# Kernel optimization log

Hardware: AMD Instinct MI355X
Metric: run time of the kernel (lower is better)

The kernel has to match this reference:

```python
import jax, jax.numpy as jnp
import numpy as np

B, QL, DL, RSZ, T = 16, 32, 12, 500, 2
DW, DH = 256, 512
HP = DH // 2  # per-direction GRU hidden
NW, NE = 50000, 100000


def _gru_dir(xp, mask, Wh, bh, reverse):
    # xp: [B, L, 3H'] precomputed input projections; mask: [B, L, 1]
    Hp = Wh.shape[1]
    xp_t = jnp.swapaxes(xp, 0, 1)
    m_t = jnp.swapaxes(mask, 0, 1)
    h0 = jnp.zeros((xp.shape[0], Hp), xp.dtype)

    def step(h, inp):
        x, m = inp
        gh = h @ Wh.T + bh
        r = jax.nn.sigmoid(x[:, :Hp] + gh[:, :Hp])
        z = jax.nn.sigmoid(x[:, Hp:2 * Hp] + gh[:, Hp:2 * Hp])
        n = jnp.tanh(x[:, 2 * Hp:] + r * gh[:, 2 * Hp:])
        hn = (1.0 - z) * n + z * h
        h = m * hn + (1.0 - m) * h  # skip updates at pad tokens
        return h, h

    hT, hs = jax.lax.scan(step, h0, (xp_t, m_t), reverse=reverse)
    return jnp.swapaxes(hs, 0, 1), hT


def _bigru(tokens, emb, Wx, Wh, bx, bh):
    # tokens: [B, L] int, 0 = pad. Wx: [2, 3H', D], Wh: [2, 3H', H'], bx/bh: [2, 3H']
    x = emb[tokens]
    mask = (tokens != 0).astype(x.dtype)[..., None]
    xp_f = jnp.einsum('bld,gd->blg', x, Wx[0]) + bx[0]
    xp_b = jnp.einsum('bld,gd->blg', x, Wx[1]) + bx[1]
    hs_f, hT_f = _gru_dir(xp_f, mask, Wh[0], bh[0], False)
    hs_b, hT_b = _gru_dir(xp_b, mask, Wh[1], bh[1], True)
    word_h = jnp.concatenate([hs_f, hs_b], -1) * mask  # zero pad positions
    sent = jnp.concatenate([hT_f, hT_b], -1)  # last fwd / last bwd hidden
    return word_h, sent


def setup_inputs() -> dict:
    key = jax.random.key(0)
    ks = jax.random.split(key, 12)

    def gru_p(k, din):
        k1, k2 = jax.random.split(k, 2)
        s = 1.0 / float(np.sqrt(HP))
        return (jax.random.normal(k1, (2, 3 * HP, din), jnp.float32) * s,
                jax.random.normal(k2, (2, 3 * HP, HP), jnp.float32) * s,
                jnp.zeros((2, 3 * HP), jnp.float32),
                jnp.zeros((2, 3 * HP), jnp.float32))

    q_Wx, q_Wh, q_bx, q_bh = gru_p(ks[0], DW)
    d_Wx, d_Wh, d_bx, d_bh = gru_p(ks[1], DW)
    kaim = float(np.sqrt(2.0 / DH))
    return {
        'questions': jax.random.randint(ks[2], (B, QL), 0, NW),
        'e_s': jax.random.uniform(ks[3], (B, NE), jnp.float32),
        'pair': jax.random.randint(ks[4], (T, B, RSZ, 2), 0, NE),
        'desc': jax.random.randint(ks[5], (T, B, RSZ, DL), 0, NW),
        'word_emb': jax.random.normal(ks[6], (NW, DW), jnp.float32) * 0.02,
        'q_Wx': q_Wx, 'q_Wh': q_Wh, 'q_bx': q_bx, 'q_bh': q_bh,
        'd_Wx': d_Wx, 'd_Wh': d_Wh, 'd_bx': d_bx, 'd_bh': d_bh,
        'step_W': jax.random.normal(ks[7], (T, DH, DH), jnp.float32) * kaim,
        'step_b': jnp.zeros((T, DH), jnp.float32),
        'rel_W': jax.random.normal(ks[8], (1, DH), jnp.float32) * kaim,
        'rel_b': jnp.zeros((1,), jnp.float32),
        'qcls_W': jax.random.normal(ks[9], (NE, DH), jnp.float32) * kaim,
        'qcls_b': jnp.zeros((NE,), jnp.float32),
    }


def reference(questions, e_s, pair, desc, word_emb, q_Wx, q_Wh, q_bx, q_bh,
              d_Wx, d_Wh, d_bx, d_bh, step_W, step_b, rel_W, rel_b, qcls_W, qcls_b):
    q_word_h, q_emb = _bigru(questions, word_emb, q_Wx, q_Wh, q_bx, q_bh)
    bsz, num_ent = e_s.shape
    last_e = e_s
    for t in range(pair.shape[0]):  # num_steps hops (small, fixed)
        cq = jnp.tanh(q_emb @ step_W[t].T + step_b[t])              # [B,H]
        q_dist = jax.nn.softmax(jnp.einsum('bh,blh->bl', cq, q_word_h), axis=1)
        ctx = jnp.einsum('bl,blh->bh', q_dist, q_word_h)            # [B,H]
        d_tok = desc[t].reshape(-1, desc.shape[-1])                 # [B*rsz, L]
        _, d_emb = _bigru(d_tok, word_emb, d_Wx, d_Wh, d_bx, d_bh)
        d_emb = d_emb.reshape(bsz, -1, d_emb.shape[-1])             # [B,rsz,H]
        d_logit = jnp.einsum('bh,brh,h->br', ctx, d_emb, rel_W[0]) + rel_b[0]
        d_prob = jax.nn.sigmoid(d_logit)                            # [B,rsz]
        sub, obj = pair[t, :, :, 0], pair[t, :, :, 1]
        obj_p = jnp.take_along_axis(last_e, sub, axis=1) * d_prob   # follow: gather
        last_e = jax.vmap(lambda o, p: jnp.zeros((num_ent,), e_s.dtype).at[o].add(p))(obj, obj_p)
        z = jax.lax.stop_gradient(jnp.where(last_e > 1.0, last_e, 1.0))
        last_e = last_e / z
    q_mask = jax.nn.sigmoid(q_emb @ qcls_W.T + qcls_b)
    return last_e * q_mask
```

## Files before the change

kernel.cpp:

```cpp
#include <hip/hip_runtime.h>
#include <math.h>

#define B_    16
#define QL_   32
#define DL_   12
#define RSZ_  500
#define T_    2
#define DW_   256
#define DH_   512
#define HP_   256
#define NW_   50000
#define NE_   100000
#define NSEQD (T_*B_*RSZ_)
#define MDESC 64
#define NBLK_DESC 500
#define NBLK_FUSED 502

typedef _Float16 half8 __attribute__((ext_vector_type(8)));
typedef float   floatx4 __attribute__((ext_vector_type(4)));

__device__ __forceinline__ float sigf(float x){
  return __builtin_amdgcn_rcpf(1.0f + __expf(-x));
}
__device__ __forceinline__ float tanhfast(float x){
  return 1.0f - 2.0f*__builtin_amdgcn_rcpf(1.0f + __expf(2.0f*x));
}

__global__ void k_prep_desc(const float* __restrict__ Wx, const float* __restrict__ Wh,
                            _Float16* __restrict__ Bd) {
  int i = blockIdx.x*256 + threadIdx.x;
  int dir = i / 393216;
  int rem = i % 393216;
  float v;
  if (rem < 262144) {
    int n = rem >> 9, k = rem & 511;
    v = (k < 256) ? Wx[(dir*768 + n)*256 + k] : Wh[(dir*768 + n)*256 + (k-256)];
  } else if (rem < 327680) {
    int r2 = rem - 262144; int j = r2 >> 8, k = r2 & 255;
    v = Wx[(dir*768 + 512 + j)*256 + k];
  } else {
    int r2 = rem - 327680; int j = r2 >> 8, k = r2 & 255;
    v = Wh[(dir*768 + 512 + j)*256 + k];
  }
  Bd[i] = (_Float16)v;
}

__global__ void k_prep_qwh(const float* __restrict__ Wh, _Float16* __restrict__ WhQ) {
  int i = blockIdx.x*256 + threadIdx.x;
  WhQ[i] = (_Float16)Wh[i];
}

__global__ void k_prep_emb16(const float* __restrict__ emb, _Float16* __restrict__ emb16) {
  int i = blockIdx.x*256 + threadIdx.x;
  const float4* s = (const float4*)emb + (size_t)i*2;
  float4 a = s[0], b = s[1];
  half8 h;
  h[0]=(_Float16)a.x; h[1]=(_Float16)a.y; h[2]=(_Float16)a.z; h[3]=(_Float16)a.w;
  h[4]=(_Float16)b.x; h[5]=(_Float16)b.y; h[6]=(_Float16)b.z; h[7]=(_Float16)b.w;
  *(half8*)(emb16 + (size_t)i*8) = h;
}

__global__ __launch_bounds__(256) void k_xproj(
    const int* __restrict__ questions, const float* __restrict__ emb,
    const float* __restrict__ Wx, const float* __restrict__ bx,
    float* __restrict__ xp)
{
  int b = blockIdx.x, n0 = blockIdx.y*128, dir = blockIdx.z;
  int tid = threadIdx.x;
  __shared__ float As[32*256];
  {
    int l = tid >> 3, c8 = tid & 7;
    int tk = questions[b*QL_ + l];
    const float4* src = (const float4*)(emb + (size_t)tk*256) + c8*8;
    float4* dst = (float4*)(As + l*256 + c8*32);
    #pragma unroll
    for (int q = 0; q < 8; ++q) dst[q] = src[q];
  }
  __syncthreads();
  int rr = tid >> 7, jj = tid & 127;
  int n = n0 + jj;
  const float4* W4 = (const float4*)(Wx + ((size_t)dir*768 + n)*256);
  const float4* A4 = (const float4*)As;
  float acc[16];
  #pragma unroll
  for (int i = 0; i < 16; ++i) acc[i] = 0.f;
  for (int k4 = 0; k4 < 64; ++k4) {
    float4 wv = W4[k4];
    #pragma unroll
    for (int i = 0; i < 16; ++i) {
      float4 av = A4[(rr*16 + i)*64 + k4];
      acc[i] += av.x*wv.x + av.y*wv.y + av.z*wv.z + av.w*wv.w;
    }
  }
  float bias = bx[dir*768 + n];
  for (int i = 0; i < 16; ++i) {
    int l = rr*16 + i;
    xp[(((size_t)dir*QL_ + l)*16 + b)*768 + n] = acc[i] + bias;
  }
}

__global__ __launch_bounds__(1024, 4) void k_fused(
    const int* __restrict__ desc, const _Float16* __restrict__ emb16,
    const _Float16* __restrict__ Bd, const float* __restrict__ dbx,
    const float* __restrict__ dbh, float* __restrict__ dh,
    const int* __restrict__ questions, const _Float16* __restrict__ WhQ,
    const float* __restrict__ qbh, const float* __restrict__ xp,
    float* __restrict__ qwh, float* __restrict__ qemb)
{
  __shared__ __align__(16) char smem[68608];
  const int bid = blockIdx.x;
  const int tid = threadIdx.x;
  const int lane = tid & 63, w = tid >> 6;
  const int lm = lane & 15, lq = lane >> 4;
  const int jl = w*16 + lm;

  if (bid < NBLK_DESC) {
    const int dir  = (bid >= 250) ? 1 : 0;
    const int seq0 = (bid - dir*250) * MDESC;
    _Float16* A2   = (_Float16*)smem;
    int*      tokA = (int*)(smem + MDESC*512*2);

    if (tid < MDESC*DL_)
      tokA[tid] = desc[(size_t)seq0*DL_ + tid];

    {
      int row = tid >> 4, cc = tid & 15;
      half8 z8 = {0,0,0,0,0,0,0,0};
      #pragma unroll
      for (int q = 0; q < 2; ++q) {
        int c = 32 + cc*2 + q;
        *(half8*)(A2 + row*512 + ((c ^ row)*8)) = z8;
      }
    }
    __syncthreads();

    const _Float16* Bdir = Bd + (size_t)dir * 393216;
    const _Float16* pR = Bdir + (size_t)jl*512;
    const _Float16* pZ = Bdir + (size_t)(256 + jl)*512;
    const _Float16* pX = Bdir + 262144 + (size_t)jl*256;
    const _Float16* pG = Bdir + 327680 + (size_t)jl*256;

    const float bias_r = dbx[dir*768 + jl]       + dbh[dir*768 + jl];
    const float bias_z = dbx[dir*768 + 256 + jl] + dbh[dir*768 + 256 + jl];
    const float bias_n = dbx[dir*768 + 512 + jl];
    const float bias_g = dbh[dir*768 + 512 + jl];

    const int l0 = dir ? (DL_-1) : 0;
    const int dl = dir ? -1 : 1;

    const int srow = tid >> 4, sp = tid & 15;
    half8 P[2];
    auto ldx = [&](int ll) {
      int tk = tokA[srow*DL_ + ll];
      const half8* src = (const half8*)(emb16 + (size_t)tk*256) + sp*2;
      P[0] = __builtin_nontemporal_load(src);
      P[1] = __builtin_nontemporal_load(src + 1);
    };
    auto stw = [&]() {
      #pragma unroll
      for (int q = 0; q < 2; ++q) {
        int c = sp*2 + q;
        *(half8*)(A2 + srow*512 + ((c ^ srow)*8)) = P[q];
      }
    };
    ldx(l0); stw();
    ldx(l0 + dl);
    __syncthreads();

    int l = l0;
    for (int t = 0; t < DL_; ++t, l += dl) {
      floatx4 accR[4], accZ[4], accN[4], accG[4];
      #pragma unroll
      for (int mi = 0; mi < 4; ++mi) {
        floatx4 z4 = {0.f,0.f,0.f,0.f};
        accR[mi]=z4; accZ[mi]=z4; accN[mi]=z4; accG[mi]=z4;
      }

      #pragma unroll
      for (int half = 0; half < 2; ++half) {
        #pragma unroll 4
        for (int kk = 0; kk < 8; ++kk) {
          int kfx = half*8 + kk;
          int k0 = kfx*32 + lq*8;
          half8 br = *(const half8*)(pR + k0);
          half8 bz = *(const half8*)(pZ + k0);
          half8 bb = half ? *(const half8*)(pG + (k0 - 256))
                          : *(const half8*)(pX + k0);
          int cb = kfx*4 + lq;
          #pragma unroll
          for (int mi = 0; mi < 4; ++mi) {
            int row = mi*16 + lm;
            half8 a = *(const half8*)(A2 + row*512 + ((cb ^ row)*8));
            accR[mi] = __builtin_amdgcn_mfma_f32_16x16x32_f16(a, br, accR[mi], 0,0,0);
            accZ[mi] = __builtin_amdgcn_mfma_f32_16x16x32_f16(a, bz, accZ[mi], 0,0,0);
            if (half) accG[mi] = __builtin_amdgcn_mfma_f32_16x16x32_f16(a, bb, accG[mi], 0,0,0);
            else      accN[mi] = __builtin_amdgcn_mfma_f32_16x16x32_f16(a, bb, accN[mi], 0,0,0);
          }
        }
      }

      __syncthreads();

      #pragma unroll
      for (int mi = 0; mi < 4; ++mi) {
        #pragma unroll
        for (int reg = 0; reg < 4; ++reg) {
          int m = mi*16 + lq*4 + reg;
          float r  = sigf(accR[mi][reg] + bias_r);
          float z  = sigf(accZ[mi][reg] + bias_z);
          float nt = tanhfast(accN[mi][reg] + bias_n + r*(accG[mi][reg] + bias_g));
          int c2 = 32 + (jl >> 3);
          _Float16* hp = A2 + m*512 + ((c2 ^ m)*8) + (jl & 7);
          float hold = (float)(*hp);
          float hn = (1.f - z)*nt + z*hold;
          int tk = tokA[m*DL_ + l];
          float hnew = (tk != 0) ? hn : hold;
          *hp = (_Float16)hnew;
          if (t == DL_-1)
            dh[((size_t)dir*NSEQD + seq0 + m)*256 + jl] = hnew;
        }
      }
      if (t < DL_-1) {
        stw();
        if (t < DL_-2) ldx(l + 2*dl);
      }
      __syncthreads();
    }
  } else {
    const int dir = bid - NBLK_DESC;
    _Float16* hA   = (_Float16*)smem;
    int*      tokS = (int*)(smem + 65536);

    if (tid < 512) {
      tokS[tid] = questions[tid];
      int row = tid >> 5, c = tid & 31;
      half8 z8 = {0,0,0,0,0,0,0,0};
      *(half8*)(hA + row*256 + ((c ^ row)*8)) = z8;
    }
    __syncthreads();

    const _Float16* pR = WhQ + ((size_t)dir*768 + jl)*256;
    const _Float16* pZ = WhQ + ((size_t)dir*768 + 256 + jl)*256;
    const _Float16* pG = WhQ + ((size_t)dir*768 + 512 + jl)*256;
    const float bh_r = qbh[dir*768 + jl];
    const float bh_z = qbh[dir*768 + 256 + jl];
    const float bh_n = qbh[dir*768 + 512 + jl];
    float hreg[4] = {0.f,0.f,0.f,0.f};

    for (int t = 0; t < QL_; ++t) {
      int l = dir ? (QL_-1-t) : t;

      float xr[4], xz[4], xn[4];
      #pragma unroll
      for (int reg = 0; reg < 4; ++reg) {
        int b = lq*4 + reg;
        const float* xb = xp + (((size_t)dir*QL_ + l)*16 + b)*768;
        xr[reg] = xb[jl];
        xz[reg] = xb[256 + jl];
        xn[reg] = xb[512 + jl];
      }

      floatx4 aR = {0,0,0,0}, aZ = {0,0,0,0}, aG = {0,0,0,0};
      #pragma unroll
      for (int kf = 0; kf < 8; ++kf) {
        int p = (kf*4 + lq) ^ lm;
        half8 a = *(const half8*)(hA + lm*256 + p*8);
        int k0 = kf*32 + lq*8;
        half8 br = *(const half8*)(pR + k0);
        half8 bz = *(const half8*)(pZ + k0);
        half8 bg = *(const half8*)(pG + k0);
        aR = __builtin_amdgcn_mfma_f32_16x16x32_f16(a, br, aR, 0,0,0);
        aZ = __builtin_amdgcn_mfma_f32_16x16x32_f16(a, bz, aZ, 0,0,0);
        aG = __builtin_amdgcn_mfma_f32_16x16x32_f16(a, bg, aG, 0,0,0);
      }
      __syncthreads();

      #pragma unroll
      for (int reg = 0; reg < 4; ++reg) {
        int b = lq*4 + reg;
        float r  = sigf(xr[reg] + aR[reg] + bh_r);
        float z  = sigf(xz[reg] + aZ[reg] + bh_z);
        float nt = tanhfast(xn[reg] + r*(aG[reg] + bh_n));
        float hold = hreg[reg];
        float hn = (1.f - z)*nt + z*hold;
        int tk = tokS[b*QL_ + l];
        float hnew = (tk != 0) ? hn : hold;
        hreg[reg] = hnew;
        int p2 = (jl >> 3) ^ b;
        hA[b*256 + p2*8 + (jl & 7)] = (_Float16)hnew;
        qwh[((size_t)b*QL_ + l)*512 + dir*256 + jl] = (tk != 0) ? hnew : 0.f;
      }
      __syncthreads();
    }
    #pragma unroll
    for (int reg = 0; reg < 4; ++reg) {
      int b = lq*4 + reg;
      qemb[b*512 + dir*256 + jl] = hreg[reg];
    }
  }
}

__global__ __launch_bounds__(256) void k_attn(
    const float* __restrict__ qemb, const float* __restrict__ qwh,
    const float* __restrict__ sW, const float* __restrict__ sb,
    const float* __restrict__ relW, float* __restrict__ u, int t)
{
  int b = blockIdx.x, tid = threadIdx.x;
  __shared__ float qe[512];
  __shared__ float cq[512];
  __shared__ float lg[32];
  __shared__ float dist[32];
  qe[tid]     = qemb[b*512 + tid];
  qe[tid+256] = qemb[b*512 + 256 + tid];
  __syncthreads();
  const float4* qe4 = (const float4*)qe;
  for (int nn = 0; nn < 2; ++nn) {
    int n = tid + nn*256;
    const float4* w4 = (const float4*)(sW + ((size_t)t*512 + n)*512);
    float acc = 0.f;
    for (int k4 = 0; k4 < 128; ++k4) {
      float4 w = w4[k4]; float4 q = qe4[k4];
      acc += w.x*q.x + w.y*q.y + w.z*q.z + w.w*q.w;
    }
    cq[n] = tanhfast(acc + sb[t*512 + n]);
  }
  __syncthreads();
  if (tid < 32) {
    const float4* r4 = (const float4*)(qwh + ((size_t)b*QL_ + tid)*512);
    const float4* c4 = (const float4*)cq;
    float acc = 0.f;
    for (int k4 = 0; k4 < 128; ++k4) {
      float4 w = r4[k4]; float4 q = c4[k4];
      acc += w.x*q.x + w.y*q.y + w.z*q.z + w.w*q.w;
    }
    lg[tid] = acc;
  }
  __syncthreads();
  if (tid == 0) {
    float mx = lg[0];
    for (int i = 1; i < 32; ++i) mx = fmaxf(mx, lg[i]);
    float s = 0.f;
    for (int i = 0; i < 32; ++i) { float e = __expf(lg[i]-mx); dist[i] = e; s += e; }
    float inv = __builtin_amdgcn_rcpf(s);
    for (int i = 0; i < 32; ++i) dist[i] *= inv;
  }
  __syncthreads();
  for (int nn = 0; nn < 2; ++nn) {
    int c = tid + nn*256;
    float acc = 0.f;
    #pragma unroll 4
    for (int ll = 0; ll < 32; ++ll)
      acc += dist[ll] * qwh[((size_t)b*QL_ + ll)*512 + c];
    u[b*512 + c] = acc * relW[c];
  }
}

__global__ __launch_bounds__(256) void k_dlogit(
    const float* __restrict__ u, const float* __restrict__ dh,
    const float* __restrict__ relb, float* __restrict__ dprob, int t)
{
  int w = threadIdx.x >> 6, lane = threadIdx.x & 63;
  int o = blockIdx.x*4 + w;
  int b = o / 500;
  int s = t*(B_*RSZ_) + o;
  const float* e0 = dh + (size_t)s*256;
  const float* e1 = dh + (size_t)NSEQD*256 + (size_t)s*256;
  float acc = 0.f;
  #pragma unroll
  for (int i = 0; i < 4; ++i) {
    int c = lane + i*64;
    acc += u[b*512 + c]       * e0[c];
    acc += u[b*512 + 256 + c] * e1[c];
  }
  #pragma unroll
  for (int off = 32; off; off >>= 1) acc += __shfl_down(acc, off);
  if (lane == 0) dprob[o] = sigf(acc + relb[0]);
}

__global__ void k_scatter(const int* __restrict__ pair, const float* __restrict__ dprob,
                          const float* __restrict__ esrc, float* __restrict__ edst,
                          int t, int clampflag)
{
  int o = blockIdx.x*256 + threadIdx.x;
  if (o >= B_*RSZ_) return;
  int b = o / RSZ_, r = o % RSZ_;
  const int* pp = pair + (((size_t)t*B_ + b)*RSZ_ + r)*2;
  int sub = pp[0], obj = pp[1];
  float v = esrc[(size_t)b*NE_ + sub];
  if (clampflag) v = fminf(v, 1.0f);
  atomicAdd(edst + (size_t)b*NE_ + obj, v * dprob[o]);
}

__global__ __launch_bounds__(256) void k_final(
    const float* __restrict__ qemb, const float* __restrict__ W,
    const float* __restrict__ bias, const float* __restrict__ efin,
    float* __restrict__ out)
{
  int tid = threadIdx.x;
  int lane = tid & 63;
  int ks = lane & 15, bg = lane >> 4;
  int b = (tid >> 6)*4 + bg;
  float q[32];
  {
    const float4* q4 = (const float4*)(qemb + b*512 + ks*32);
    #pragma unroll
    for (int i = 0; i < 8; ++i) {
      float4 v = q4[i];
      q[4*i]=v.x; q[4*i+1]=v.y; q[4*i+2]=v.z; q[4*i+3]=v.w;
    }
  }
  int e0 = blockIdx.x*256;
  int eend = (e0+256 < NE_) ? e0+256 : NE_;
  for (int e = e0; e < eend; e += 2) {
    const float4* w4a = (const float4*)(W + (size_t)e*512 + ks*32);
    const float4* w4b = (const float4*)(W + (size_t)(e+1)*512 + ks*32);
    float acca = 0.f, accb = 0.f;
    #pragma unroll
    for (int i = 0; i < 8; ++i) {
      float4 va = w4a[i];
      float4 vb = w4b[i];
      acca += va.x*q[4*i] + va.y*q[4*i+1] + va.z*q[4*i+2] + va.w*q[4*i+3];
      accb += vb.x*q[4*i] + vb.y*q[4*i+1] + vb.z*q[4*i+2] + vb.w*q[4*i+3];
    }
    acca += __shfl_xor(acca, 1); accb += __shfl_xor(accb, 1);
    acca += __shfl_xor(acca, 2); accb += __shfl_xor(accb, 2);
    acca += __shfl_xor(acca, 4); accb += __shfl_xor(accb, 4);
    acca += __shfl_xor(acca, 8); accb += __shfl_xor(accb, 8);
    if (ks == 0) {
      float mska = sigf(acca + bias[e]);
      float eva  = fminf(efin[(size_t)b*NE_ + e], 1.0f);
      out[(size_t)b*NE_ + e] = eva * mska;
      float mskb = sigf(accb + bias[e+1]);
      float evb  = fminf(efin[(size_t)b*NE_ + e+1], 1.0f);
      out[(size_t)b*NE_ + e+1] = evb * mskb;
    }
  }
}

extern "C" void kernel_launch(void* const* d_in, const int* in_sizes, int n_in,
                              void* d_out, int out_size, void* d_ws, size_t ws_size,
                              hipStream_t stream)
{
  const int*   questions = (const int*)d_in[0];
  const float* e_s   = (const float*)d_in[1];
  const int*   pair  = (const int*)d_in[2];
  const int*   desc  = (const int*)d_in[3];
  const float* emb   = (const float*)d_in[4];
  const float* qWx   = (const float*)d_in[5];
  const float* qWh   = (const float*)d_in[6];
  const float* qbx   = (const float*)d_in[7];
  const float* qbh   = (const float*)d_in[8];
  const float* dWx   = (const float*)d_in[9];
  const float* dWh   = (const float*)d_in[10];
  const float* dbx   = (const float*)d_in[11];
  const float* dbh   = (const float*)d_in[12];
  const float* stepW = (const float*)d_in[13];
  const float* stepb = (const float*)d_in[14];
  const float* relW  = (const float*)d_in[15];
  const float* relb  = (const float*)d_in[16];
  const float* qclsW = (const float*)d_in[17];
  const float* qclsb = (const float*)d_in[18];
  float* out = (float*)d_out;

  char* ws = (char*)d_ws;
  size_t off = 0;
  auto alloc = [&](size_t bytes)->void* {
    void* p = ws + off; off += (bytes + 255) & ~(size_t)255; return p;
  };
  _Float16* Bd   = (_Float16*)alloc((size_t)2*393216*sizeof(_Float16));
  _Float16* WhQ  = (_Float16*)alloc((size_t)2*768*256*sizeof(_Float16));
  _Float16* emb16= (_Float16*)alloc((size_t)NW_*256*sizeof(_Float16));
  float* xp   = (float*)alloc((size_t)2*QL_*16*768*sizeof(float));
  float* qemb = (float*)alloc((size_t)16*512*sizeof(float));
  float* qwh  = (float*)alloc((size_t)16*QL_*512*sizeof(float));
  float* dh   = (float*)alloc((size_t)2*NSEQD*256*sizeof(float));
  float* u    = (float*)alloc((size_t)16*512*sizeof(float));
  float* dprob= (float*)alloc((size_t)B_*RSZ_*sizeof(float));
  float* ebuf = (float*)emb16;

  k_prep_desc<<<3072, 256, 0, stream>>>(dWx, dWh, Bd);
  k_prep_qwh<<<1536, 256, 0, stream>>>(qWh, WhQ);
  k_prep_emb16<<<6250, 256, 0, stream>>>(emb, emb16);

  k_xproj<<<dim3(16,6,2), 256, 0, stream>>>(questions, emb, qWx, qbx, xp);

  k_fused<<<NBLK_FUSED, 1024, 0, stream>>>(desc, emb16, Bd, dbx, dbh, dh,
                                           questions, WhQ, qbh, xp, qwh, qemb);

  hipMemsetAsync(ebuf, 0, (size_t)2*B_*NE_*sizeof(float), stream);

  for (int t = 0; t < T_; ++t) {
    k_attn<<<16, 256, 0, stream>>>(qemb, qwh, stepW, stepb, relW, u, t);
    k_dlogit<<<2000, 256, 0, stream>>>(u, dh, relb, dprob, t);
    const float* esrc = (t == 0) ? e_s : ebuf;
    float* edst = ebuf + (size_t)t*B_*NE_;
    k_scatter<<<32, 256, 0, stream>>>(pair, dprob, esrc, edst, t, t);
  }
  k_final<<<(NE_+255)/256, 256, 0, stream>>>(qemb, qclsW, qclsb, ebuf + (size_t)B_*NE_, out);
}
```

Baseline: 1.766 ms.

## Enlarge desc GRU tile to 128 sequences with 512 threads, two column tiles per wave

Each desc block now processes 128 sequences with 512 threads, so every wave computes two 16-column output tiles over 8 row tiles. Each weight fragment loaded from global is reused across twice as many rows. The gate GEMMs are split into R/G, N and Z phases to limit live accumulators, and the old h values are kept packed in registers instead of being reread from LDS. The embedding prefetch for the next step is issued after the barrier rather than a step ahead. The costs are a 137KB LDS footprint, which allows only one block per CU, half as many blocks (252) for the GPU, and high register pressure.

```diff
diff --git a/kernel.cpp b/kernel.cpp
--- a/kernel.cpp
+++ b/kernel.cpp
@@ -12,9 +12,9 @@
 #define NW_   50000
 #define NE_   100000
 #define NSEQD (T_*B_*RSZ_)
-#define MDESC 64
-#define NBLK_DESC 500
-#define NBLK_FUSED 502
+#define MDESC 128
+#define NBLK_DESC 250
+#define NBLK_FUSED 252
 
 typedef _Float16 half8 __attribute__((ext_vector_type(8)));
 typedef float   floatx4 __attribute__((ext_vector_type(4)));
@@ -99,7 +99,7 @@
   }
 }
 
-__global__ __launch_bounds__(1024, 4) void k_fused(
+__global__ __launch_bounds__(512, 2) void k_fused(
     const int* __restrict__ desc, const _Float16* __restrict__ emb16,
     const _Float16* __restrict__ Bd, const float* __restrict__ dbx,
     const float* __restrict__ dbh, float* __restrict__ dh,
@@ -107,196 +107,308 @@
     const float* __restrict__ qbh, const float* __restrict__ xp,
     float* __restrict__ qwh, float* __restrict__ qemb)
 {
-  __shared__ __align__(16) char smem[68608];
+  __shared__ __align__(16) char smem[137216];
   const int bid = blockIdx.x;
   const int tid = threadIdx.x;
   const int lane = tid & 63, w = tid >> 6;
   const int lm = lane & 15, lq = lane >> 4;
   const int jl = w*16 + lm;
+  const int jl2 = jl + 128;
 
   if (bid < NBLK_DESC) {
-    const int dir  = (bid >= 250) ? 1 : 0;
-    const int seq0 = (bid - dir*250) * MDESC;
+    const int dir  = (bid >= 125) ? 1 : 0;
+    const int seq0 = (bid - dir*125) * MDESC;
     _Float16* A2   = (_Float16*)smem;
     int*      tokA = (int*)(smem + MDESC*512*2);
 
-    if (tid < MDESC*DL_)
-      tokA[tid] = desc[(size_t)seq0*DL_ + tid];
+    for (int i = tid; i < MDESC*DL_; i += 512)
+      tokA[i] = desc[(size_t)seq0*DL_ + i];
 
     {
-      int row = tid >> 4, cc = tid & 15;
+      int row = tid >> 2, cc = tid & 3;
       half8 z8 = {0,0,0,0,0,0,0,0};
       #pragma unroll
-      for (int q = 0; q < 2; ++q) {
-        int c = 32 + cc*2 + q;
-        *(half8*)(A2 + row*512 + ((c ^ row)*8)) = z8;
+      for (int q = 0; q < 8; ++q) {
+        int c = 32 + cc*8 + q;
+        *(half8*)(A2 + row*512 + ((c ^ (row & 63))*8)) = z8;
       }
     }
     __syncthreads();
 
     const _Float16* Bdir = Bd + (size_t)dir * 393216;
-    const _Float16* pR = Bdir + (size_t)jl*512;
-    const _Float16* pZ = Bdir + (size_t)(256 + jl)*512;
-    const _Float16* pX = Bdir + 262144 + (size_t)jl*256;
-    const _Float16* pG = Bdir + 327680 + (size_t)jl*256;
-
-    const float bias_r = dbx[dir*768 + jl]       + dbh[dir*768 + jl];
-    const float bias_z = dbx[dir*768 + 256 + jl] + dbh[dir*768 + 256 + jl];
-    const float bias_n = dbx[dir*768 + 512 + jl];
-    const float bias_g = dbh[dir*768 + 512 + jl];
+    const _Float16* pR1 = Bdir + (size_t)jl *512;
+    const _Float16* pR2 = Bdir + (size_t)jl2*512;
+    const _Float16* pZ1 = Bdir + (size_t)(256 + jl )*512;
+    const _Float16* pZ2 = Bdir + (size_t)(256 + jl2)*512;
+    const _Float16* pX1 = Bdir + 262144 + (size_t)jl *256;
+    const _Float16* pX2 = Bdir + 262144 + (size_t)jl2*256;
+    const _Float16* pG1 = Bdir + 327680 + (size_t)jl *256;
+    const _Float16* pG2 = Bdir + 327680 + (size_t)jl2*256;
+
+    const float bias_r1 = dbx[dir*768 + jl ]       + dbh[dir*768 + jl ];
+    const float bias_r2 = dbx[dir*768 + jl2]       + dbh[dir*768 + jl2];
+    const float bias_z1 = dbx[dir*768 + 256 + jl ] + dbh[dir*768 + 256 + jl ];
+    const float bias_z2 = dbx[dir*768 + 256 + jl2] + dbh[dir*768 + 256 + jl2];
+    const float bias_n1 = dbx[dir*768 + 512 + jl ];
+    const float bias_n2 = dbx[dir*768 + 512 + jl2];
+    const float bias_g1 = dbh[dir*768 + 512 + jl ];
+    const float bias_g2 = dbh[dir*768 + 512 + jl2];
 
     const int l0 = dir ? (DL_-1) : 0;
     const int dl = dir ? -1 : 1;
 
-    const int srow = tid >> 4, sp = tid & 15;
-    half8 P[2];
+    const int srow = tid >> 2, sp = tid & 3;
+    half8 P[8];
     auto ldx = [&](int ll) {
       int tk = tokA[srow*DL_ + ll];
-      const half8* src = (const half8*)(emb16 + (size_t)tk*256) + sp*2;
-      P[0] = __builtin_nontemporal_load(src);
-      P[1] = __builtin_nontemporal_load(src + 1);
+      const half8* src = (const half8*)(emb16 + (size_t)tk*256) + sp*8;
+      #pragma unroll
+      for (int q = 0; q < 8; ++q) P[q] = __builtin_nontemporal_load(src + q);
     };
     auto stw = [&]() {
       #pragma unroll
-      for (int q = 0; q < 2; ++q) {
-        int c = sp*2 + q;
-        *(half8*)(A2 + srow*512 + ((c ^ srow)*8)) = P[q];
+      for (int q = 0; q < 8; ++q) {
+        int c = sp*8 + q;
+        *(half8*)(A2 + srow*512 + ((c ^ (srow & 63))*8)) = P[q];
       }
     };
     ldx(l0); stw();
-    ldx(l0 + dl);
     __syncthreads();
+
+    unsigned h2[8][4];
+    #pragma unroll
+    for (int mi = 0; mi < 8; ++mi)
+      #pragma unroll
+      for (int reg = 0; reg < 4; ++reg) h2[mi][reg] = 0u;
 
     int l = l0;
     for (int t = 0; t < DL_; ++t, l += dl) {
-      floatx4 accR[4], accZ[4], accN[4], accG[4];
-      #pragma unroll
-      for (int mi = 0; mi < 4; ++mi) {
+      floatx4 accR[8][2], accG[8][2];
+      {
         floatx4 z4 = {0.f,0.f,0.f,0.f};
-        accR[mi]=z4; accZ[mi]=z4; accN[mi]=z4; accG[mi]=z4;
-      }
-
-      #pragma unroll
-      for (int half = 0; half < 2; ++half) {
-        #pragma unroll 4
-        for (int kk = 0; kk < 8; ++kk) {
-          int kfx = half*8 + kk;
-          int k0 = kfx*32 + lq*8;
-          half8 br = *(const half8*)(pR + k0);
-          half8 bz = *(const half8*)(pZ + k0);
-          half8 bb = half ? *(const half8*)(pG + (k0 - 256))
-                          : *(const half8*)(pX + k0);
-          int cb = kfx*4 + lq;
+        #pragma unroll
+        for (int mi = 0; mi < 8; ++mi) {
+          accR[mi][0]=z4; accR[mi][1]=z4; accG[mi][0]=z4; accG[mi][1]=z4;
+        }
+      }
+      #pragma unroll
+      for (int kfx = 0; kfx < 16; ++kfx) {
+        int k0 = kfx*32 + lq*8;
+        half8 br1 = *(const half8*)(pR1 + k0);
+        half8 br2 = *(const half8*)(pR2 + k0);
+        half8 bg1, bg2;
+        if (kfx >= 8) {
+          int kg = (kfx-8)*32 + lq*8;
+          bg1 = *(const half8*)(pG1 + kg);
+          bg2 = *(const half8*)(pG2 + kg);
+        }
+        int cb = kfx*4 + lq;
+        #pragma unroll
+        for (int mi = 0; mi < 8; ++mi) {
+          int row = mi*16 + lm;
+          half8 a = *(const half8*)(A2 + row*512 + ((cb ^ (row & 63))*8));
+          accR[mi][0] = __builtin_amdgcn_mfma_f32_16x16x32_f16(a, br1, accR[mi][0], 0,0,0);
+          accR[mi][1] = __builtin_amdgcn_mfma_f32_16x16x32_f16(a, br2, accR[mi][1], 0,0,0);
+          if (kfx >= 8) {
+            accG[mi][0] = __builtin_amdgcn_mfma_f32_16x16x32_f16(a, bg1, accG[mi][0], 0,0,0);
+            accG[mi][1] = __builtin_amdgcn_mfma_f32_16x16x32_f16(a, bg2, accG[mi][1], 0,0,0);
+          }
+        }
+      }
+      floatx4 tp[8][2];
+      #pragma unroll
+      for (int mi = 0; mi < 8; ++mi)
+        #pragma unroll
+        for (int nt = 0; nt < 2; ++nt)
           #pragma unroll
-          for (int mi = 0; mi < 4; ++mi) {
-            int row = mi*16 + lm;
-            half8 a = *(const half8*)(A2 + row*512 + ((cb ^ row)*8));
-            accR[mi] = __builtin_amdgcn_mfma_f32_16x16x32_f16(a, br, accR[mi], 0,0,0);
-            accZ[mi] = __builtin_amdgcn_mfma_f32_16x16x32_f16(a, bz, accZ[mi], 0,0,0);
-            if (half) accG[mi] = __builtin_amdgcn_mfma_f32_16x16x32_f16(a, bb, accG[mi], 0,0,0);
-            else      accN[mi] = __builtin_amdgcn_mfma_f32_16x16x32_f16(a, bb, accN[mi], 0,0,0);
+          for (int e = 0; e < 4; ++e) {
+            float r = sigf(accR[mi][nt][e] + (nt ? bias_r2 : bias_r1));
+            tp[mi][nt][e] = r * (accG[mi][nt][e] + (nt ? bias_g2 : bias_g1));
           }
+
+      floatx4 accN[8][2];
+      {
+        floatx4 z4 = {0.f,0.f,0.f,0.f};
+        #pragma unroll
+        for (int mi = 0; mi < 8; ++mi) { accN[mi][0]=z4; accN[mi][1]=z4; }
+      }
+      #pragma unroll
+      for (int kfx = 0; kfx < 8; ++kfx) {
+        int k0 = kfx*32 + lq*8;
+        half8 bx1 = *(const half8*)(pX1 + k0);
+        half8 bx2 = *(const half8*)(pX2 + k0);
+        int cb = kfx*4 + lq;
+        #pragma unroll
+        for (int mi = 0; mi < 8; ++mi) {
+          int row = mi*16 + lm;
+          half8 a = *(const half8*)(A2 + row*512 + ((cb ^ (row & 63))*8));
+          accN[mi][0] = __builtin_amdgcn_mfma_f32_16x16x32_f16(a, bx1, accN[mi][0], 0,0,0);
+          accN[mi][1] = __builtin_amdgcn_mfma_f32_16x16x32_f16(a, bx2, accN[mi][1], 0,0,0);
+        }
+      }
+      #pragma unroll
+      for (int mi = 0; mi < 8; ++mi)
+        #pragma unroll
+        for (int nt = 0; nt < 2; ++nt)
+          #pragma unroll
+          for (int e = 0; e < 4; ++e)
+            tp[mi][nt][e] = tanhfast(accN[mi][nt][e] + (nt ? bias_n2 : bias_n1) + tp[mi][nt][e]);
+
+      floatx4 accZ[8][2];
+      {
+        floatx4 z4 = {0.f,0.f,0.f,0.f};
+        #pragma unroll
+        for (int mi = 0; mi < 8; ++mi) { accZ[mi][0]=z4; accZ[mi][1]=z4; }
+      }
+      #pragma unroll
+      for (int kfx = 0; kfx < 16; ++kfx) {
+        int k0 = kfx*32 + lq*8;
+        half8 bz1 = *(const half8*)(pZ1 + k0);
+        half8 bz2 = *(const half8*)(pZ2 + k0);
+        int cb = kfx*4 + lq;
+        #pragma unroll
+        for (int mi = 0; mi < 8; ++mi) {
+          int row = mi*16 + lm;
+          half8 a = *(const half8*)(A2 + row*512 + ((cb ^ (row & 63))*8));
+          accZ[mi][0] = __builtin_amdgcn_mfma_f32_16x16x32_f16(a, bz1, accZ[mi][0], 0,0,0);
+          accZ[mi][1] = __builtin_amdgcn_mfma_f32_16x16x32_f16(a, bz2, accZ[mi][1], 0,0,0);
         }
       }
 
       __syncthreads();
 
-      #pragma unroll
-      for (int mi = 0; mi < 4; ++mi) {
+      if (t < DL_-1) ldx(l + dl);
+
+      #pragma unroll
+      for (int mi = 0; mi < 8; ++mi) {
         #pragma unroll
         for (int reg = 0; reg < 4; ++reg) {
           int m = mi*16 + lq*4 + reg;
-          float r  = sigf(accR[mi][reg] + bias_r);
-          float z  = sigf(accZ[mi][reg] + bias_z);
-          float nt = tanhfast(accN[mi][reg] + bias_n + r*(accG[mi][reg] + bias_g));
-          int c2 = 32 + (jl >> 3);
-          _Float16* hp = A2 + m*512 + ((c2 ^ m)*8) + (jl & 7);
-          float hold = (float)(*hp);
-          float hn = (1.f - z)*nt + z*hold;
           int tk = tokA[m*DL_ + l];
-          float hnew = (tk != 0) ? hn : hold;
-          *hp = (_Float16)hnew;
-          if (t == DL_-1)
-            dh[((size_t)dir*NSEQD + seq0 + m)*256 + jl] = hnew;
-        }
-      }
-      if (t < DL_-1) {
-        stw();
-        if (t < DL_-2) ldx(l + 2*dl);
-      }
+          unsigned hp = h2[mi][reg];
+          unsigned hpn = 0u;
+          #pragma unroll
+          for (int nt = 0; nt < 2; ++nt) {
+            int j = nt ? jl2 : jl;
+            unsigned short ub = nt ? (unsigned short)(hp >> 16)
+                                   : (unsigned short)(hp & 0xFFFFu);
+            float hold = (float)__builtin_bit_cast(_Float16, ub);
+            float z  = sigf(accZ[mi][nt][reg] + (nt ? bias_z2 : bias_z1));
+            float nv = tp[mi][nt][reg];
+            float hn = (1.f - z)*nv + z*hold;
+            float hnew = (tk != 0) ? hn : hold;
+            _Float16 h16 = (_Float16)hnew;
+            int c2 = 32 + (j >> 3);
+            A2[m*512 + ((c2 ^ (m & 63))*8) + (j & 7)] = h16;
+            if (t == DL_-1)
+              dh[((size_t)dir*NSEQD + seq0 + m)*256 + j] = hnew;
+            unsigned short nb = __builtin_bit_cast(unsigned short, h16);
+            hpn |= nt ? ((unsigned)nb << 16) : (unsigned)nb;
+          }
+          h2[mi][reg] = hpn;
+        }
+      }
+      if (t < DL_-1) stw();
       __syncthreads();
     }
   } else {
     const int dir = bid - NBLK_DESC;
     _Float16* hA   = (_Float16*)smem;
-    int*      tokS = (int*)(smem + 65536);
-
-    if (tid < 512) {
-      tokS[tid] = questions[tid];
+    int*      tokS = (int*)(smem + 8192);
+
+    tokS[tid] = questions[tid];
+    {
       int row = tid >> 5, c = tid & 31;
       half8 z8 = {0,0,0,0,0,0,0,0};
       *(half8*)(hA + row*256 + ((c ^ row)*8)) = z8;
     }
     __syncthreads();
 
-    const _Float16* pR = WhQ + ((size_t)dir*768 + jl)*256;
-    const _Float16* pZ = WhQ + ((size_t)dir*768 + 256 + jl)*256;
-    const _Float16* pG = WhQ + ((size_t)dir*768 + 512 + jl)*256;
-    const float bh_r = qbh[dir*768 + jl];
-    const float bh_z = qbh[dir*768 + 256 + jl];
-    const float bh_n = qbh[dir*768 + 512 + jl];
-    float hreg[4] = {0.f,0.f,0.f,0.f};
+    const _Float16* pR1 = WhQ + ((size_t)dir*768 + jl )*256;
+    const _Float16* pR2 = WhQ + ((size_t)dir*768 + jl2)*256;
+    const _Float16* pZ1 = WhQ + ((size_t)dir*768 + 256 + jl )*256;
+    const _Float16* pZ2 = WhQ + ((size_t)dir*768 + 256 + jl2)*256;
+    const _Float16* pG1 = WhQ + ((size_t)dir*768 + 512 + jl )*256;
+    const _Float16* pG2 = WhQ + ((size_t)dir*768 + 512 + jl2)*256;
+    const float bh_r1 = qbh[dir*768 + jl ],       bh_r2 = qbh[dir*768 + jl2];
+    const float bh_z1 = qbh[dir*768 + 256 + jl ], bh_z2 = qbh[dir*768 + 256 + jl2];
+    const float bh_n1 = qbh[dir*768 + 512 + jl ], bh_n2 = qbh[dir*768 + 512 + jl2];
+
+    float hreg[2][4];
+    #pragma unroll
+    for (int nt = 0; nt < 2; ++nt)
+      #pragma unroll
+      for (int reg = 0; reg < 4; ++reg) hreg[nt][reg] = 0.f;
 
     for (int t = 0; t < QL_; ++t) {
       int l = dir ? (QL_-1-t) : t;
 
-      float xr[4], xz[4], xn[4];
-      #pragma unroll
-      for (int reg = 0; reg < 4; ++reg) {
-        int b = lq*4 + reg;
-        const float* xb = xp + (((size_t)dir*QL_ + l)*16 + b)*768;
-        xr[reg] = xb[jl];
-        xz[reg] = xb[256 + jl];
-        xn[reg] = xb[512 + jl];
-      }
-
-      floatx4 aR = {0,0,0,0}, aZ = {0,0,0,0}, aG = {0,0,0,0};
+      float xr[2][4], xz[2][4], xn[2][4];
+      #pragma unroll
+      for (int nt = 0; nt < 2; ++nt)
+        #pragma unroll
+        for (int reg = 0; reg < 4; ++reg) {
+          int b = lq*4 + reg;
+          int j = nt ? jl2 : jl;
+          const float* xb = xp + (((size_t)dir*QL_ + l)*16 + b)*768;
+          xr[nt][reg] = xb[j];
+          xz[nt][reg] = xb[256 + j];
+          xn[nt][reg] = xb[512 + j];
+        }
+
+      floatx4 aR[2], aZ[2], aG[2];
+      {
+        floatx4 z4 = {0.f,0.f,0.f,0.f};
+        aR[0]=z4; aR[1]=z4; aZ[0]=z4; aZ[1]=z4; aG[0]=z4; aG[1]=z4;
+      }
       #pragma unroll
       for (int kf = 0; kf < 8; ++kf) {
         int p = (kf*4 + lq) ^ lm;
         half8 a = *(const half8*)(hA + lm*256 + p*8);
         int k0 = kf*32 + lq*8;
-        half8 br = *(const half8*)(pR + k0);
-        half8 bz = *(const half8*)(pZ + k0);
-        half8 bg = *(const half8*)(pG + k0);
-        aR = __builtin_amdgcn_mfma_f32_16x16x32_f16(a, br, aR, 0,0,0);
-        aZ = __builtin_amdgcn_mfma_f32_16x16x32_f16(a, bz, aZ, 0,0,0);
-        aG = __builtin_amdgcn_mfma_f32_16x16x32_f16(a, bg, aG, 0,0,0);
+        half8 br1 = *(const half8*)(pR1 + k0);
+        half8 br2 = *(const half8*)(pR2 + k0);
+        half8 bz1 = *(const half8*)(pZ1 + k0);
+        half8 bz2 = *(const half8*)(pZ2 + k0);
+        half8 bg1 = *(const half8*)(pG1 + k0);
+        half8 bg2 = *(const half8*)(pG2 + k0);
+        aR[0] = __builtin_amdgcn_mfma_f32_16x16x32_f16(a, br1, aR[0], 0,0,0);
+        aR[1] = __builtin_amdgcn_mfma_f32_16x16x32_f16(a, br2, aR[1], 0,0,0);
+        aZ[0] = __builtin_amdgcn_mfma_f32_16x16x32_f16(a, bz1, aZ[0], 0,0,0);
+        aZ[1] = __builtin_amdgcn_mfma_f32_16x16x32_f16(a, bz2, aZ[1], 0,0,0);
+        aG[0] = __builtin_amdgcn_mfma_f32_16x16x32_f16(a, bg1, aG[0], 0,0,0);
+        aG[1] = __builtin_amdgcn_mfma_f32_16x16x32_f16(a, bg2, aG[1], 0,0,0);
       }
       __syncthreads();
 
+      #pragma unroll
+      for (int nt = 0; nt < 2; ++nt)
+        #pragma unroll
+        for (int reg = 0; reg < 4; ++reg) {
+          int b = lq*4 + reg;
+          int j = nt ? jl2 : jl;
+          float r  = sigf(xr[nt][reg] + aR[nt][reg] + (nt ? bh_r2 : bh_r1));
+          float z  = sigf(xz[nt][reg] + aZ[nt][reg] + (nt ? bh_z2 : bh_z1));
+          float nv = tanhfast(xn[nt][reg] + r*(aG[nt][reg] + (nt ? bh_n2 : bh_n1)));
+          float hold = hreg[nt][reg];
+          float hn = (1.f - z)*nv + z*hold;
+          int tk = tokS[b*QL_ + l];
+          float hnew = (tk != 0) ? hn : hold;
+          hreg[nt][reg] = hnew;
+          int p2 = (j >> 3) ^ b;
+          hA[b*256 + p2*8 + (j & 7)] = (_Float16)hnew;
+          qwh[((size_t)b*QL_ + l)*512 + dir*256 + j] = (tk != 0) ? hnew : 0.f;
+        }
+      __syncthreads();
+    }
+    #pragma unroll
+    for (int nt = 0; nt < 2; ++nt)
       #pragma unroll
       for (int reg = 0; reg < 4; ++reg) {
         int b = lq*4 + reg;
-        float r  = sigf(xr[reg] + aR[reg] + bh_r);
-        float z  = sigf(xz[reg] + aZ[reg] + bh_z);
-        float nt = tanhfast(xn[reg] + r*(aG[reg] + bh_n));
-        float hold = hreg[reg];
-        float hn = (1.f - z)*nt + z*hold;
-        int tk = tokS[b*QL_ + l];
-        float hnew = (tk != 0) ? hn : hold;
-        hreg[reg] = hnew;
-        int p2 = (jl >> 3) ^ b;
-        hA[b*256 + p2*8 + (jl & 7)] = (_Float16)hnew;
-        qwh[((size_t)b*QL_ + l)*512 + dir*256 + jl] = (tk != 0) ? hnew : 0.f;
-      }
-      __syncthreads();
-    }
-    #pragma unroll
-    for (int reg = 0; reg < 4; ++reg) {
-      int b = lq*4 + reg;
-      qemb[b*512 + dir*256 + jl] = hreg[reg];
-    }
+        int j = nt ? jl2 : jl;
+        qemb[b*512 + dir*256 + j] = hreg[nt][reg];
+      }
   }
 }
 
@@ -484,8 +596,8 @@
 
   k_xproj<<<dim3(16,6,2), 256, 0, stream>>>(questions, emb, qWx, qbx, xp);
 
-  k_fused<<<NBLK_FUSED, 1024, 0, stream>>>(desc, emb16, Bd, dbx, dbh, dh,
-                                           questions, WhQ, qbh, xp, qwh, qemb);
+  k_fused<<<NBLK_FUSED, 512, 0, stream>>>(desc, emb16, Bd, dbx, dbh, dh,
+                                          questions, WhQ, qbh, xp, qwh, qemb);
 
   hipMemsetAsync(ebuf, 0, (size_t)2*B_*NE_*sizeof(float), stream);
 
```

Result: slower. 2.551 ms (+44.4%).
